# Kernel optimization log

Measured on AMD Instinct MI355X. Metric: run time of the kernel, lower is better.

The kernel has to match this reference:

```python
import jax, jax.numpy as jnp
import numpy as np

B, T, FBINS = 256, 512, 128
L1, L2, L3, NCLASS = 256, 256, 128, 10
Q_SCALE = 8.0  # 4-bit fixed point in [-1, 1]


def _quant(w):
    return jnp.clip(jnp.round(w * Q_SCALE) / Q_SCALE, -1.0, 1.0)


def qw(w):
    # straight-through quantizer (identity gradient)
    return w + jax.lax.stop_gradient(_quant(w) - w)


def egru_cell(x, h, W, b, H):
    # eGRU: 2-gate cell (update gate + candidate), softsign activations
    a = jnp.concatenate([x, h], axis=-1) @ qw(W).T + b  # [B, 2H]
    z = 0.5 * (jax.nn.soft_sign(a[:, :H]) + 1.0)
    h_cand = jax.nn.soft_sign(a[:, H:])
    return z * h + (1.0 - z) * h_cand


def setup_inputs() -> dict:
    key = jax.random.key(0)
    ks = jax.random.split(key, 8)
    s = lambda fan_in: 1.0 / np.sqrt(fan_in)
    return {
        "inputs": jax.random.normal(ks[0], (B, T, FBINS), jnp.float32),
        "h1_init": jax.random.uniform(ks[1], (B, L1), jnp.float32, -1.0, 1.0),
        "h2_init": jax.random.uniform(ks[2], (B, L2), jnp.float32, -1.0, 1.0),
        "W1": jax.random.normal(ks[3], (2 * L1, FBINS + L1), jnp.float32) * s(FBINS + L1),
        "b1": jnp.zeros((2 * L1,), jnp.float32),
        "W2": jax.random.normal(ks[4], (2 * L2, L1 + L2), jnp.float32) * s(L1 + L2),
        "b2": jnp.zeros((2 * L2,), jnp.float32),
        "W3": jax.random.normal(ks[5], (L3, L2), jnp.float32) * s(L2),
        "b3": jnp.zeros((L3,), jnp.float32),
        "W4": jax.random.normal(ks[6], (NCLASS, L3), jnp.float32) * s(L3),
        "b4": jnp.zeros((NCLASS,), jnp.float32),
    }


def reference(inputs, h1_init, h2_init, W1, b1, W2, b2, W3, b3, W4, b4):
    def step(carry, x_t):
        h1, h2 = carry
        h1 = egru_cell(x_t, h1, W1, b1, L1)
        h2 = egru_cell(h1, h2, W2, b2, L2)
        h3 = jnp.maximum(h2 @ qw(W3).T + b3, 0.0)  # clamp(min=0)
        h4 = h3 @ qw(W4).T + b4
        return (h1, h2), h4

    xs = jnp.swapaxes(inputs, 0, 1)  # [T, B, F]
    _, ys = jax.lax.scan(step, (h1_init, h2_init), xs)  # [T, B, C]
    y = jnp.swapaxes(ys, 0, 1)  # [B, T, C]
    return jax.nn.log_softmax(y, axis=-1)
```

## Files before the change

### kernel.cpp

```cpp
#include <hip/hip_runtime.h>

#define NT 512
#define FB 128
#define HD 256
#define NC 10
#define NG 32
#define GR 8

typedef __attribute__((ext_vector_type(8))) short bf16x8;
typedef __attribute__((ext_vector_type(4))) float f32x4;
typedef __attribute__((ext_vector_type(4))) unsigned u32x4;
typedef __attribute__((ext_vector_type(2))) unsigned u32x2;

static __device__ __forceinline__ short f2bf(float f){
  union { float f; unsigned u; } v; v.f = f;
  return (short)((v.u + 0x7fffu + ((v.u >> 16) & 1u)) >> 16);
}
static __device__ __forceinline__ float bf2f(short h){
  union { unsigned u; float f; } v; v.u = ((unsigned)(unsigned short)h) << 16;
  return v.f;
}
static __device__ __forceinline__ float quantw(float w){
  return fminf(fmaxf(rintf(w * 8.0f) * 0.125f, -1.0f), 1.0f);
}
static __device__ __forceinline__ bf16x8 loadqw8(const float* __restrict__ p){
  bf16x8 v;
#pragma unroll
  for (int j = 0; j < 8; ++j) v[j] = f2bf(quantw(p[j]));
  return v;
}
static __device__ __forceinline__ void split8(f32x4 a, f32x4 b, bf16x8& hi, bf16x8& lo){
  float v0[4] = {a[0],a[1],a[2],a[3]}, v1[4] = {b[0],b[1],b[2],b[3]};
#pragma unroll
  for (int j = 0; j < 4; ++j){
    short h = f2bf(v0[j]); hi[j] = h; lo[j] = f2bf(v0[j] - bf2f(h));
  }
#pragma unroll
  for (int j = 0; j < 4; ++j){
    short h = f2bf(v1[j]); hi[4+j] = h; lo[4+j] = f2bf(v1[j] - bf2f(h));
  }
}

static __device__ __forceinline__ void st_msg(unsigned* p, short hb, short lb, unsigned ep){
  u32x2 w;
  w[0] = (((unsigned)(unsigned short)hb) << 16) | ep;
  w[1] = (((unsigned)(unsigned short)lb) << 16) | ep;
  asm volatile("global_store_dwordx2 %0, %1, off sc1" :: "v"(p), "v"(w) : "memory");
}
static __device__ __forceinline__ void gather8(const unsigned* p, unsigned ep, bf16x8& hv, bf16x8& lv){
  u32x4 a, b, c, d;
  for (;;){
    asm volatile("global_load_dwordx4 %0, %4, off sc1\n\t"
                 "global_load_dwordx4 %1, %4, off offset:16 sc1\n\t"
                 "global_load_dwordx4 %2, %4, off offset:32 sc1\n\t"
                 "global_load_dwordx4 %3, %4, off offset:48 sc1\n\t"
                 "s_waitcnt vmcnt(0)"
                 : "=&v"(a), "=&v"(b), "=&v"(c), "=&v"(d) : "v"(p) : "memory");
    unsigned m = (a[0]^ep)|(a[1]^ep)|(a[2]^ep)|(a[3]^ep)
               | (b[0]^ep)|(b[1]^ep)|(b[2]^ep)|(b[3]^ep)
               | (c[0]^ep)|(c[1]^ep)|(c[2]^ep)|(c[3]^ep)
               | (d[0]^ep)|(d[1]^ep)|(d[2]^ep)|(d[3]^ep);
    if ((m & 0xffffu) == 0u) break;
  }
  hv[0]=(short)(a[0]>>16); lv[0]=(short)(a[1]>>16);
  hv[1]=(short)(a[2]>>16); lv[1]=(short)(a[3]>>16);
  hv[2]=(short)(b[0]>>16); lv[2]=(short)(b[1]>>16);
  hv[3]=(short)(b[2]>>16); lv[3]=(short)(b[3]>>16);
  hv[4]=(short)(c[0]>>16); lv[4]=(short)(c[1]>>16);
  hv[5]=(short)(c[2]>>16); lv[5]=(short)(c[3]>>16);
  hv[6]=(short)(d[0]>>16); lv[6]=(short)(d[1]>>16);
  hv[7]=(short)(d[2]>>16); lv[7]=(short)(d[3]>>16);
}

__global__ __launch_bounds__(256, 1)
void egru_persistent(const float* __restrict__ xg,
                     const float* __restrict__ h1ig, const float* __restrict__ h2ig,
                     const float* __restrict__ W1g, const float* __restrict__ b1g,
                     const float* __restrict__ W2g, const float* __restrict__ b2g,
                     const float* __restrict__ W3g, const float* __restrict__ b3g,
                     const float* __restrict__ W4g, const float* __restrict__ b4g,
                     float* __restrict__ outg, float* __restrict__ wsf)
{
  const int tid = threadIdx.x;
  const int gp  = blockIdx.x & 31;
  const int sb  = blockIdx.x >> 5;
  const int wv  = tid >> 6;
  const int ln  = tid & 15;
  const int lk  = (tid >> 4) & 3;
  const int rz  = sb * 32;
  const int lnl = 8 + (ln & 7);

  __shared__ __align__(16) short in1[16*384];
  __shared__ __align__(16) short in2[16*512];
  __shared__ float aldsA[64][17];
  __shared__ float aldsB[64][17];
  __shared__ float h1own[32][GR];
  __shared__ float h2own[32][GR];
  __shared__ float h3p[128], h3q[128], h3row[128];
  __shared__ float ytmp[16];
  __shared__ float W4L[10*130];
  __shared__ float b1s[64], b2s[64], b3L[128], b4L[10];

  unsigned* h1buf = reinterpret_cast<unsigned*>(wsf);
  unsigned* h2buf = h1buf + 262144;

  bf16x8 w1f[12], w2f[16], w3f[2][8];
  {
    const int arow = (wv < 2) ? (rz + wv*16 + ln) : (256 + rz + (wv-2)*16 + ln);
#pragma unroll
    for (int ks = 0; ks < 12; ++ks) w1f[ks] = loadqw8(W1g + arow*384 + ks*32 + lk*8);
#pragma unroll
    for (int ks = 0; ks < 16; ++ks) w2f[ks] = loadqw8(W2g + arow*512 + ks*32 + lk*8);
#pragma unroll
    for (int tl = 0; tl < 2; ++tl)
#pragma unroll
      for (int ks = 0; ks < 8; ++ks)
        w3f[tl][ks] = loadqw8(W3g + (wv*32 + tl*16 + ln)*256 + ks*32 + lk*8);
  }

  if (tid < 64){
    int grow = (tid < 32) ? (rz + tid) : (256 + rz + (tid - 32));
    b1s[tid] = b1g[grow];
    b2s[tid] = b2g[grow];
  }
  if (tid < 128) b3L[tid] = b3g[tid];
  if (tid < 10)  b4L[tid] = b4g[tid];
  for (int i = tid; i < 1280; i += 256)
    W4L[(i >> 7)*130 + (i & 127)] = quantw(W4g[i]);

  const int ur = tid >> 5, uc = tid & 31;
  {
    bf16x8 hv, lv;
    const float* p1 = h1ig + (size_t)(gp*GR + ur)*HD + uc*8;
    split8(*(const f32x4*)p1, *(const f32x4*)(p1+4), hv, lv);
    *(bf16x8*)((char*)in1 + ur*768       + ((256 + uc*16) ^ ((ur&7)<<4))) = hv;
    *(bf16x8*)((char*)in1 + (ur+8)*768   + ((256 + uc*16) ^ ((ur&7)<<4))) = lv;
    *(bf16x8*)((char*)in2 + ur*1024      + ((      uc*16) ^ ((ur&7)<<4))) = hv;
    *(bf16x8*)((char*)in2 + (ur+8)*1024  + ((      uc*16) ^ ((ur&7)<<4))) = lv;
    const float* p2 = h2ig + (size_t)(gp*GR + ur)*HD + uc*8;
    split8(*(const f32x4*)p2, *(const f32x4*)(p2+4), hv, lv);
    *(bf16x8*)((char*)in2 + ur*1024      + ((512 + uc*16) ^ ((ur&7)<<4))) = hv;
    *(bf16x8*)((char*)in2 + (ur+8)*1024  + ((512 + uc*16) ^ ((ur&7)<<4))) = lv;
    h1own[uc][ur] = h1ig[(size_t)(gp*GR+ur)*HD + rz + uc];
    h2own[uc][ur] = h2ig[(size_t)(gp*GR+ur)*HD + rz + uc];
  }
  const int xr = tid >> 4, xf = tid & 15;
  if (xr < 8){
    const float* px = xg + ((size_t)(gp*GR + xr)*NT + 0)*FB + xf*8;
    bf16x8 hv, lv;
    split8(*(const f32x4*)px, *(const f32x4*)(px+4), hv, lv);
    *(bf16x8*)((char*)in1 + xr*768     + ((xf*16) ^ ((xr&7)<<4))) = hv;
    *(bf16x8*)((char*)in1 + (xr+8)*768 + ((xf*16) ^ ((xr&7)<<4))) = lv;
  }
  __syncthreads();

  f32x4 acc1 = {0.f,0.f,0.f,0.f};
#pragma unroll
  for (int ks = 0; ks < 12; ++ks){
    bf16x8 bfr = *(bf16x8*)((char*)in1 + ln*768 + ((ks*64 + lk*16) ^ ((ln&7)<<4)));
    acc1 = __builtin_amdgcn_mfma_f32_16x16x32_bf16(w1f[ks], bfr, acc1, 0, 0, 0);
  }

  for (int t = 0; t < NT; ++t){
    unsigned* h1s = h1buf + (unsigned)(t & 1)*131072u + (unsigned)(gp*GR)*512u;
    unsigned* h2s = h2buf + (unsigned)(t & 1)*131072u + (unsigned)(gp*GR)*512u;
    unsigned* h2r = h2buf + (unsigned)((t + 1) & 1)*131072u + (unsigned)(gp*GR)*512u;

#pragma unroll
    for (int r4 = 0; r4 < 4; ++r4)
      aldsA[wv*16 + lk*4 + r4][ln] = acc1[r4];
    __syncthreads();
    {
      float az = aldsA[uc][ur]    + aldsA[uc][ur+8]    + b1s[uc];
      float ac = aldsA[32+uc][ur] + aldsA[32+uc][ur+8] + b1s[32+uc];
      float z  = 0.5f*(az/(1.0f+fabsf(az)) + 1.0f);
      float cd = ac/(1.0f+fabsf(ac));
      float hn = z*h1own[uc][ur] + (1.0f - z)*cd;
      h1own[uc][ur] = hn;
      short hb = f2bf(hn), lb = f2bf(hn - bf2f(hb));
      st_msg(&h1s[ur*512 + (rz + uc)*2], hb, lb, (unsigned)(t+1));
    }

    f32x4 xa = {0,0,0,0}, xb = {0,0,0,0};
    const bool pf = ((t+1) < NT) && (xr < 8);
    if (pf){
      const float* px = xg + ((size_t)(gp*GR + xr)*NT + (t+1))*FB + xf*8;
      xa = *(const f32x4*)px; xb = *(const f32x4*)(px+4);
    }

    if (t > 0){
      bf16x8 hv, lv;
      gather8(&h2r[ur*512 + uc*16], (unsigned)t, hv, lv);
      *(bf16x8*)((char*)in2 + ur*1024     + ((512 + uc*16) ^ ((ur&7)<<4))) = hv;
      *(bf16x8*)((char*)in2 + (ur+8)*1024 + ((512 + uc*16) ^ ((ur&7)<<4))) = lv;
    }
    if (pf){
      bf16x8 hv, lv;
      split8(xa, xb, hv, lv);
      *(bf16x8*)((char*)in1 + xr*768     + ((xf*16) ^ ((xr&7)<<4))) = hv;
      *(bf16x8*)((char*)in1 + (xr+8)*768 + ((xf*16) ^ ((xr&7)<<4))) = lv;
    }
    __syncthreads();

    f32x4 acc2 = {0.f,0.f,0.f,0.f};
#pragma unroll
    for (int ks = 8; ks < 16; ++ks){
      bf16x8 bfr = *(bf16x8*)((char*)in2 + ln*1024 + ((ks*64 + lk*16) ^ ((ln&7)<<4)));
      acc2 = __builtin_amdgcn_mfma_f32_16x16x32_bf16(w2f[ks], bfr, acc2, 0, 0, 0);
    }
    if (t > 0){
      f32x4 acc3a = {0,0,0,0}, acc3b = {0,0,0,0};
#pragma unroll
      for (int ks = 0; ks < 8; ++ks){
        bf16x8 bfr = *(bf16x8*)((char*)in2 + ln*1024 + ((512 + ks*64 + lk*16) ^ ((ln&7)<<4)));
        acc3a = __builtin_amdgcn_mfma_f32_16x16x32_bf16(w3f[0][ks], bfr, acc3a, 0, 0, 0);
        acc3b = __builtin_amdgcn_mfma_f32_16x16x32_bf16(w3f[1][ks], bfr, acc3b, 0, 0, 0);
      }
      if (ln == sb){
#pragma unroll
        for (int r4 = 0; r4 < 4; ++r4){
          int d0 = wv*32 + lk*4 + r4;
          h3p[d0] = acc3a[r4]; h3p[d0+16] = acc3b[r4];
        }
      }
      if (ln == sb + 8){
#pragma unroll
        for (int r4 = 0; r4 < 4; ++r4){
          int d0 = wv*32 + lk*4 + r4;
          h3q[d0] = acc3a[r4]; h3q[d0+16] = acc3b[r4];
        }
      }
      __syncthreads();
      if (tid < 128) h3row[tid] = fmaxf(h3p[tid] + h3q[tid] + b3L[tid], 0.0f);
      __syncthreads();
      if (wv == 0){
        const int l = tid, c = l >> 2, kq = l & 3;
        float p = 0.f;
        if (c < 10){
          const float* wr = &W4L[c*130 + kq*32];
          const float* hr = &h3row[kq*32];
#pragma unroll
          for (int k = 0; k < 32; ++k) p += wr[k]*hr[k];
        }
        p += __shfl_xor(p, 1, 4);
        p += __shfl_xor(p, 2, 4);
        if (c < 10 && kq == 0) ytmp[c] = p + b4L[c];
        asm volatile("s_waitcnt lgkmcnt(0)" ::: "memory");
        float yv = (l < 10) ? ytmp[l] : -INFINITY;
        float mx = yv;
#pragma unroll
        for (int off = 1; off < 16; off <<= 1)
          mx = fmaxf(mx, __shfl_xor(mx, off, 16));
        float ex = (l < 10) ? expf(yv - mx) : 0.0f;
        float sm = ex;
#pragma unroll
        for (int off = 1; off < 16; off <<= 1)
          sm += __shfl_xor(sm, off, 16);
        if (l < 10)
          outg[((size_t)(gp*GR + sb)*NT + (t-1))*NC + l] = yv - (mx + logf(sm));
      }
    }

    {
      bf16x8 hv, lv;
      gather8(&h1s[ur*512 + uc*16], (unsigned)(t+1), hv, lv);
      *(bf16x8*)((char*)in1 + ur*768      + ((256 + uc*16) ^ ((ur&7)<<4))) = hv;
      *(bf16x8*)((char*)in1 + (ur+8)*768  + ((256 + uc*16) ^ ((ur&7)<<4))) = lv;
      *(bf16x8*)((char*)in2 + ur*1024     + ((      uc*16) ^ ((ur&7)<<4))) = hv;
      *(bf16x8*)((char*)in2 + (ur+8)*1024 + ((      uc*16) ^ ((ur&7)<<4))) = lv;
    }
    __syncthreads();

#pragma unroll
    for (int ks = 0; ks < 8; ++ks){
      bf16x8 bfr = *(bf16x8*)((char*)in2 + ln*1024 + ((ks*64 + lk*16) ^ ((ln&7)<<4)));
      acc2 = __builtin_amdgcn_mfma_f32_16x16x32_bf16(w2f[ks], bfr, acc2, 0, 0, 0);
    }
#pragma unroll
    for (int r4 = 0; r4 < 4; ++r4)
      aldsB[wv*16 + lk*4 + r4][ln] = acc2[r4];
    __syncthreads();
    {
      float az = aldsB[uc][ur]    + aldsB[uc][ur+8]    + b2s[uc];
      float ac = aldsB[32+uc][ur] + aldsB[32+uc][ur+8] + b2s[32+uc];
      float z  = 0.5f*(az/(1.0f+fabsf(az)) + 1.0f);
      float cd = ac/(1.0f+fabsf(ac));
      float hn = z*h2own[uc][ur] + (1.0f - z)*cd;
      h2own[uc][ur] = hn;
      short hb = f2bf(hn), lb = f2bf(hn - bf2f(hb));
      st_msg(&h2s[ur*512 + (rz + uc)*2], hb, lb, (unsigned)(t+1));
    }

    if (t + 1 < NT){
      f32x4 a1n = {0.f,0.f,0.f,0.f};
#pragma unroll
      for (int ks = 0; ks < 12; ++ks){
        bf16x8 bfr = *(bf16x8*)((char*)in1 + ln*768 + ((ks*64 + lk*16) ^ ((ln&7)<<4)));
        a1n = __builtin_amdgcn_mfma_f32_16x16x32_bf16(w1f[ks], bfr, a1n, 0, 0, 0);
      }
      acc1 = a1n;
    }
  }

  {
    unsigned* h2e = h2buf + (unsigned)((NT-1) & 1)*131072u + (unsigned)(gp*GR)*512u;
    bf16x8 hv, lv;
    gather8(&h2e[ur*512 + uc*16], (unsigned)NT, hv, lv);
    *(bf16x8*)((char*)in2 + ur*1024     + ((512 + uc*16) ^ ((ur&7)<<4))) = hv;
    *(bf16x8*)((char*)in2 + (ur+8)*1024 + ((512 + uc*16) ^ ((ur&7)<<4))) = lv;
  }
  __syncthreads();
  {
    f32x4 acc3a = {0,0,0,0}, acc3b = {0,0,0,0};
#pragma unroll
    for (int ks = 0; ks < 8; ++ks){
      bf16x8 bfr = *(bf16x8*)((char*)in2 + ln*1024 + ((512 + ks*64 + lk*16) ^ ((ln&7)<<4)));
      acc3a = __builtin_amdgcn_mfma_f32_16x16x32_bf16(w3f[0][ks], bfr, acc3a, 0, 0, 0);
      acc3b = __builtin_amdgcn_mfma_f32_16x16x32_bf16(w3f[1][ks], bfr, acc3b, 0, 0, 0);
    }
    if (ln == sb){
#pragma unroll
      for (int r4 = 0; r4 < 4; ++r4){
        int d0 = wv*32 + lk*4 + r4;
        h3p[d0] = acc3a[r4]; h3p[d0+16] = acc3b[r4];
      }
    }
    if (ln == sb + 8){
#pragma unroll
      for (int r4 = 0; r4 < 4; ++r4){
        int d0 = wv*32 + lk*4 + r4;
        h3q[d0] = acc3a[r4]; h3q[d0+16] = acc3b[r4];
      }
    }
    __syncthreads();
    if (tid < 128) h3row[tid] = fmaxf(h3p[tid] + h3q[tid] + b3L[tid], 0.0f);
    __syncthreads();
    if (wv == 0){
      const int l = tid, c = l >> 2, kq = l & 3;
      float p = 0.f;
      if (c < 10){
        const float* wr = &W4L[c*130 + kq*32];
        const float* hr = &h3row[kq*32];
#pragma unroll
        for (int k = 0; k < 32; ++k) p += wr[k]*hr[k];
      }
      p += __shfl_xor(p, 1, 4);
      p += __shfl_xor(p, 2, 4);
      if (c < 10 && kq == 0) ytmp[c] = p + b4L[c];
      asm volatile("s_waitcnt lgkmcnt(0)" ::: "memory");
      float yv = (l < 10) ? ytmp[l] : -INFINITY;
      float mx = yv;
#pragma unroll
      for (int off = 1; off < 16; off <<= 1)
        mx = fmaxf(mx, __shfl_xor(mx, off, 16));
      float ex = (l < 10) ? expf(yv - mx) : 0.0f;
      float sm = ex;
#pragma unroll
      for (int off = 1; off < 16; off <<= 1)
        sm += __shfl_xor(sm, off, 16);
      if (l < 10)
        outg[((size_t)(gp*GR + sb)*NT + (NT-1))*NC + l] = yv - (mx + logf(sm));
    }
  }
}

extern "C" void kernel_launch(void* const* d_in, const int* in_sizes, int n_in,
                              void* d_out, int out_size, void* d_ws, size_t ws_size,
                              hipStream_t stream) {
  const float* xg  = (const float*)d_in[0];
  const float* h1i = (const float*)d_in[1];
  const float* h2i = (const float*)d_in[2];
  const float* W1  = (const float*)d_in[3];
  const float* b1  = (const float*)d_in[4];
  const float* W2  = (const float*)d_in[5];
  const float* b2  = (const float*)d_in[6];
  const float* W3  = (const float*)d_in[7];
  const float* b3  = (const float*)d_in[8];
  const float* W4  = (const float*)d_in[9];
  const float* b4  = (const float*)d_in[10];
  float* out = (float*)d_out;
  float* ws  = (float*)d_ws;

  hipMemsetAsync(d_ws, 0, 2u * 1024u * 1024u, stream);

  egru_persistent<<<dim3(256), dim3(256), 0, stream>>>(
      xg, h1i, h2i, W1, b1, W2, b2, W3, b3, W4, b4, out, ws);
}
```

Before: 1.904 ms.

## Issue cross-block hidden-state polls early and overlap with compute in persistent eGRU

The h2 and h1 message loads and the next-step x prefetch are now issued asynchronously ahead of use, with explicit vmcnt waits and a fallback spin loop if the epoch tags are not ready yet. This is meant to hide global-memory round-trip latency on the per-step critical path. Shared input buffers are split into separate x/h1/h2 arrays, h2 fragments are loaded once and reused for both W2 and W3 MFMAs, and h1 fragments are reused for the next W1 step. __syncthreads is replaced with a raw barrier macro and W4 LDS padding is changed, which adds reliance on hand-managed wait counts and scheduling barriers.

```diff
diff --git a/kernel.cpp b/kernel.cpp
--- a/kernel.cpp
+++ b/kernel.cpp
@@ -10,7 +10,6 @@
 typedef __attribute__((ext_vector_type(8))) short bf16x8;
 typedef __attribute__((ext_vector_type(4))) float f32x4;
 typedef __attribute__((ext_vector_type(4))) unsigned u32x4;
-typedef __attribute__((ext_vector_type(2))) unsigned u32x2;
 
 static __device__ __forceinline__ short f2bf(float f){
   union { float f; unsigned u; } v; v.f = f;
@@ -42,7 +41,7 @@
 }
 
 static __device__ __forceinline__ void st_msg(unsigned* p, short hb, short lb, unsigned ep){
-  u32x2 w;
+  __attribute__((ext_vector_type(2))) unsigned w;
   w[0] = (((unsigned)(unsigned short)hb) << 16) | ep;
   w[1] = (((unsigned)(unsigned short)lb) << 16) | ep;
   asm volatile("global_store_dwordx2 %0, %1, off sc1" :: "v"(p), "v"(w) : "memory");
@@ -71,6 +70,42 @@
   hv[6]=(short)(d[0]>>16); lv[6]=(short)(d[1]>>16);
   hv[7]=(short)(d[2]>>16); lv[7]=(short)(d[3]>>16);
 }
+static __device__ __forceinline__ bool chk_unpack(u32x4 a, u32x4 b, u32x4 c, u32x4 d,
+                                                  unsigned ep, bf16x8& hv, bf16x8& lv){
+  unsigned m = (a[0]^ep)|(a[1]^ep)|(a[2]^ep)|(a[3]^ep)
+             | (b[0]^ep)|(b[1]^ep)|(b[2]^ep)|(b[3]^ep)
+             | (c[0]^ep)|(c[1]^ep)|(c[2]^ep)|(c[3]^ep)
+             | (d[0]^ep)|(d[1]^ep)|(d[2]^ep)|(d[3]^ep);
+  if ((m & 0xffffu) != 0u) return false;
+  hv[0]=(short)(a[0]>>16); lv[0]=(short)(a[1]>>16);
+  hv[1]=(short)(a[2]>>16); lv[1]=(short)(a[3]>>16);
+  hv[2]=(short)(b[0]>>16); lv[2]=(short)(b[1]>>16);
+  hv[3]=(short)(b[2]>>16); lv[3]=(short)(b[3]>>16);
+  hv[4]=(short)(c[0]>>16); lv[4]=(short)(c[1]>>16);
+  hv[5]=(short)(c[2]>>16); lv[5]=(short)(c[3]>>16);
+  hv[6]=(short)(d[0]>>16); lv[6]=(short)(d[1]>>16);
+  hv[7]=(short)(d[2]>>16); lv[7]=(short)(d[3]>>16);
+  return true;
+}
+
+#define ISSUE_G8(P,A,B,C,D) \
+  asm volatile("global_load_dwordx4 %0, %4, off sc1\n\t" \
+               "global_load_dwordx4 %1, %4, off offset:16 sc1\n\t" \
+               "global_load_dwordx4 %2, %4, off offset:32 sc1\n\t" \
+               "global_load_dwordx4 %3, %4, off offset:48 sc1" \
+               : "=&v"(A),"=&v"(B),"=&v"(C),"=&v"(D) : "v"(P) : "memory")
+#define ISSUE_X2(P,A,B) \
+  asm volatile("global_load_dwordx4 %0, %2, off\n\t" \
+               "global_load_dwordx4 %1, %2, off offset:16" \
+               : "=&v"(A),"=&v"(B) : "v"(P) : "memory")
+#define WAITV4(N,A,B,C,D) do{ \
+  asm volatile("s_waitcnt vmcnt(" #N ")" : "+v"(A),"+v"(B),"+v"(C),"+v"(D) :: "memory"); \
+  __builtin_amdgcn_sched_barrier(0); }while(0)
+#define WAITV2(N,A,B) do{ \
+  asm volatile("s_waitcnt vmcnt(" #N ")" : "+v"(A),"+v"(B) :: "memory"); \
+  __builtin_amdgcn_sched_barrier(0); }while(0)
+#define BARRIER() do{ asm volatile("s_waitcnt lgkmcnt(0)" ::: "memory"); \
+  __builtin_amdgcn_s_barrier(); asm volatile("" ::: "memory"); }while(0)
 
 __global__ __launch_bounds__(256, 1)
 void egru_persistent(const float* __restrict__ xg,
@@ -88,17 +123,17 @@
   const int ln  = tid & 15;
   const int lk  = (tid >> 4) & 3;
   const int rz  = sb * 32;
-  const int lnl = 8 + (ln & 7);
-
-  __shared__ __align__(16) short in1[16*384];
-  __shared__ __align__(16) short in2[16*512];
+
+  __shared__ __align__(16) short inX [16*128];
+  __shared__ __align__(16) short inH1[16*256];
+  __shared__ __align__(16) short inH2[16*256];
   __shared__ float aldsA[64][17];
   __shared__ float aldsB[64][17];
   __shared__ float h1own[32][GR];
   __shared__ float h2own[32][GR];
   __shared__ float h3p[128], h3q[128], h3row[128];
   __shared__ float ytmp[16];
-  __shared__ float W4L[10*130];
+  __shared__ float W4L[1344];
   __shared__ float b1s[64], b2s[64], b3L[128], b4L[10];
 
   unsigned* h1buf = reinterpret_cast<unsigned*>(wsf);
@@ -125,22 +160,22 @@
   }
   if (tid < 128) b3L[tid] = b3g[tid];
   if (tid < 10)  b4L[tid] = b4g[tid];
-  for (int i = tid; i < 1280; i += 256)
-    W4L[(i >> 7)*130 + (i & 127)] = quantw(W4g[i]);
+  for (int i = tid; i < 1280; i += 256){
+    int c = i >> 7, k = i & 127;
+    W4L[c*134 + (k>>5)*33 + (k&31)] = quantw(W4g[i]);
+  }
 
   const int ur = tid >> 5, uc = tid & 31;
   {
     bf16x8 hv, lv;
     const float* p1 = h1ig + (size_t)(gp*GR + ur)*HD + uc*8;
     split8(*(const f32x4*)p1, *(const f32x4*)(p1+4), hv, lv);
-    *(bf16x8*)((char*)in1 + ur*768       + ((256 + uc*16) ^ ((ur&7)<<4))) = hv;
-    *(bf16x8*)((char*)in1 + (ur+8)*768   + ((256 + uc*16) ^ ((ur&7)<<4))) = lv;
-    *(bf16x8*)((char*)in2 + ur*1024      + ((      uc*16) ^ ((ur&7)<<4))) = hv;
-    *(bf16x8*)((char*)in2 + (ur+8)*1024  + ((      uc*16) ^ ((ur&7)<<4))) = lv;
+    *(bf16x8*)((char*)inH1 + ur*512     + ((uc*16) ^ ((ur&7)<<4))) = hv;
+    *(bf16x8*)((char*)inH1 + (ur+8)*512 + ((uc*16) ^ ((ur&7)<<4))) = lv;
     const float* p2 = h2ig + (size_t)(gp*GR + ur)*HD + uc*8;
     split8(*(const f32x4*)p2, *(const f32x4*)(p2+4), hv, lv);
-    *(bf16x8*)((char*)in2 + ur*1024      + ((512 + uc*16) ^ ((ur&7)<<4))) = hv;
-    *(bf16x8*)((char*)in2 + (ur+8)*1024  + ((512 + uc*16) ^ ((ur&7)<<4))) = lv;
+    *(bf16x8*)((char*)inH2 + ur*512     + ((uc*16) ^ ((ur&7)<<4))) = hv;
+    *(bf16x8*)((char*)inH2 + (ur+8)*512 + ((uc*16) ^ ((ur&7)<<4))) = lv;
     h1own[uc][ur] = h1ig[(size_t)(gp*GR+ur)*HD + rz + uc];
     h2own[uc][ur] = h2ig[(size_t)(gp*GR+ur)*HD + rz + uc];
   }
@@ -149,16 +184,21 @@
     const float* px = xg + ((size_t)(gp*GR + xr)*NT + 0)*FB + xf*8;
     bf16x8 hv, lv;
     split8(*(const f32x4*)px, *(const f32x4*)(px+4), hv, lv);
-    *(bf16x8*)((char*)in1 + xr*768     + ((xf*16) ^ ((xr&7)<<4))) = hv;
-    *(bf16x8*)((char*)in1 + (xr+8)*768 + ((xf*16) ^ ((xr&7)<<4))) = lv;
+    *(bf16x8*)((char*)inX + xr*256     + ((xf*16) ^ ((xr&7)<<4))) = hv;
+    *(bf16x8*)((char*)inX + (xr+8)*256 + ((xf*16) ^ ((xr&7)<<4))) = lv;
   }
   __syncthreads();
 
   f32x4 acc1 = {0.f,0.f,0.f,0.f};
 #pragma unroll
-  for (int ks = 0; ks < 12; ++ks){
-    bf16x8 bfr = *(bf16x8*)((char*)in1 + ln*768 + ((ks*64 + lk*16) ^ ((ln&7)<<4)));
-    acc1 = __builtin_amdgcn_mfma_f32_16x16x32_bf16(w1f[ks], bfr, acc1, 0, 0, 0);
+  for (int j = 0; j < 4; ++j){
+    bf16x8 fx = *(bf16x8*)((char*)inX + ln*256 + ((j*64 + lk*16) ^ ((ln&7)<<4)));
+    acc1 = __builtin_amdgcn_mfma_f32_16x16x32_bf16(w1f[j], fx, acc1, 0, 0, 0);
+  }
+#pragma unroll
+  for (int j = 0; j < 8; ++j){
+    bf16x8 fh = *(bf16x8*)((char*)inH1 + ln*512 + ((j*64 + lk*16) ^ ((ln&7)<<4)));
+    acc1 = __builtin_amdgcn_mfma_f32_16x16x32_bf16(w1f[4+j], fh, acc1, 0, 0, 0);
   }
 
   for (int t = 0; t < NT; ++t){
@@ -166,10 +206,13 @@
     unsigned* h2s = h2buf + (unsigned)(t & 1)*131072u + (unsigned)(gp*GR)*512u;
     unsigned* h2r = h2buf + (unsigned)((t + 1) & 1)*131072u + (unsigned)(gp*GR)*512u;
 
+    u32x4 g2a, g2b, g2c, g2d;
+    if (t > 0) ISSUE_G8(&h2r[ur*512 + uc*16], g2a, g2b, g2c, g2d);
+
 #pragma unroll
     for (int r4 = 0; r4 < 4; ++r4)
       aldsA[wv*16 + lk*4 + r4][ln] = acc1[r4];
-    __syncthreads();
+    BARRIER();
     {
       float az = aldsA[uc][ur]    + aldsA[uc][ur+8]    + b1s[uc];
       float ac = aldsA[32+uc][ur] + aldsA[32+uc][ur+8] + b1s[32+uc];
@@ -181,40 +224,41 @@
       st_msg(&h1s[ur*512 + (rz + uc)*2], hb, lb, (unsigned)(t+1));
     }
 
+    if (t > 0){
+      WAITV4(1, g2a, g2b, g2c, g2d);
+      bf16x8 hv, lv;
+      if (!chk_unpack(g2a, g2b, g2c, g2d, (unsigned)t, hv, lv))
+        gather8(&h2r[ur*512 + uc*16], (unsigned)t, hv, lv);
+      *(bf16x8*)((char*)inH2 + ur*512     + ((uc*16) ^ ((ur&7)<<4))) = hv;
+      *(bf16x8*)((char*)inH2 + (ur+8)*512 + ((uc*16) ^ ((ur&7)<<4))) = lv;
+    }
+
+    u32x4 g1a, g1b, g1c, g1d;
+    ISSUE_G8(&h1s[ur*512 + uc*16], g1a, g1b, g1c, g1d);
     f32x4 xa = {0,0,0,0}, xb = {0,0,0,0};
     const bool pf = ((t+1) < NT) && (xr < 8);
     if (pf){
       const float* px = xg + ((size_t)(gp*GR + xr)*NT + (t+1))*FB + xf*8;
-      xa = *(const f32x4*)px; xb = *(const f32x4*)(px+4);
-    }
-
-    if (t > 0){
-      bf16x8 hv, lv;
-      gather8(&h2r[ur*512 + uc*16], (unsigned)t, hv, lv);
-      *(bf16x8*)((char*)in2 + ur*1024     + ((512 + uc*16) ^ ((ur&7)<<4))) = hv;
-      *(bf16x8*)((char*)in2 + (ur+8)*1024 + ((512 + uc*16) ^ ((ur&7)<<4))) = lv;
-    }
-    if (pf){
-      bf16x8 hv, lv;
-      split8(xa, xb, hv, lv);
-      *(bf16x8*)((char*)in1 + xr*768     + ((xf*16) ^ ((xr&7)<<4))) = hv;
-      *(bf16x8*)((char*)in1 + (xr+8)*768 + ((xf*16) ^ ((xr&7)<<4))) = lv;
-    }
-    __syncthreads();
-
+      ISSUE_X2(px, xa, xb);
+    }
+    BARRIER();
+
+    bf16x8 fh2[8];
+#pragma unroll
+    for (int j = 0; j < 8; ++j)
+      fh2[j] = *(bf16x8*)((char*)inH2 + ln*512 + ((j*64 + lk*16) ^ ((ln&7)<<4)));
     f32x4 acc2 = {0.f,0.f,0.f,0.f};
 #pragma unroll
-    for (int ks = 8; ks < 16; ++ks){
-      bf16x8 bfr = *(bf16x8*)((char*)in2 + ln*1024 + ((ks*64 + lk*16) ^ ((ln&7)<<4)));
-      acc2 = __builtin_amdgcn_mfma_f32_16x16x32_bf16(w2f[ks], bfr, acc2, 0, 0, 0);
-    }
+    for (int j = 0; j < 8; ++j)
+      acc2 = __builtin_amdgcn_mfma_f32_16x16x32_bf16(w2f[8+j], fh2[j], acc2, 0, 0, 0);
+
+    float outv = 0.f; bool dow = false; size_t oaddr = 0;
     if (t > 0){
       f32x4 acc3a = {0,0,0,0}, acc3b = {0,0,0,0};
 #pragma unroll
-      for (int ks = 0; ks < 8; ++ks){
-        bf16x8 bfr = *(bf16x8*)((char*)in2 + ln*1024 + ((512 + ks*64 + lk*16) ^ ((ln&7)<<4)));
-        acc3a = __builtin_amdgcn_mfma_f32_16x16x32_bf16(w3f[0][ks], bfr, acc3a, 0, 0, 0);
-        acc3b = __builtin_amdgcn_mfma_f32_16x16x32_bf16(w3f[1][ks], bfr, acc3b, 0, 0, 0);
+      for (int j = 0; j < 8; ++j){
+        acc3a = __builtin_amdgcn_mfma_f32_16x16x32_bf16(w3f[0][j], fh2[j], acc3a, 0, 0, 0);
+        acc3b = __builtin_amdgcn_mfma_f32_16x16x32_bf16(w3f[1][j], fh2[j], acc3b, 0, 0, 0);
       }
       if (ln == sb){
 #pragma unroll
@@ -230,14 +274,14 @@
           h3q[d0] = acc3a[r4]; h3q[d0+16] = acc3b[r4];
         }
       }
-      __syncthreads();
+      BARRIER();
       if (tid < 128) h3row[tid] = fmaxf(h3p[tid] + h3q[tid] + b3L[tid], 0.0f);
-      __syncthreads();
+      BARRIER();
       if (wv == 0){
         const int l = tid, c = l >> 2, kq = l & 3;
         float p = 0.f;
         if (c < 10){
-          const float* wr = &W4L[c*130 + kq*32];
+          const float* wr = &W4L[c*134 + kq*33];
           const float* hr = &h3row[kq*32];
 #pragma unroll
           for (int k = 0; k < 32; ++k) p += wr[k]*hr[k];
@@ -256,30 +300,36 @@
 #pragma unroll
         for (int off = 1; off < 16; off <<= 1)
           sm += __shfl_xor(sm, off, 16);
-        if (l < 10)
-          outg[((size_t)(gp*GR + sb)*NT + (t-1))*NC + l] = yv - (mx + logf(sm));
+        if (l < 10){
+          outv = yv - (mx + logf(sm));
+          dow = true;
+          oaddr = ((size_t)(gp*GR + sb)*NT + (t-1))*NC + l;
+        }
       }
     }
 
     {
+      WAITV4(2, g1a, g1b, g1c, g1d);
       bf16x8 hv, lv;
-      gather8(&h1s[ur*512 + uc*16], (unsigned)(t+1), hv, lv);
-      *(bf16x8*)((char*)in1 + ur*768      + ((256 + uc*16) ^ ((ur&7)<<4))) = hv;
-      *(bf16x8*)((char*)in1 + (ur+8)*768  + ((256 + uc*16) ^ ((ur&7)<<4))) = lv;
-      *(bf16x8*)((char*)in2 + ur*1024     + ((      uc*16) ^ ((ur&7)<<4))) = hv;
-      *(bf16x8*)((char*)in2 + (ur+8)*1024 + ((      uc*16) ^ ((ur&7)<<4))) = lv;
-    }
-    __syncthreads();
-
-#pragma unroll
-    for (int ks = 0; ks < 8; ++ks){
-      bf16x8 bfr = *(bf16x8*)((char*)in2 + ln*1024 + ((ks*64 + lk*16) ^ ((ln&7)<<4)));
-      acc2 = __builtin_amdgcn_mfma_f32_16x16x32_bf16(w2f[ks], bfr, acc2, 0, 0, 0);
-    }
+      if (!chk_unpack(g1a, g1b, g1c, g1d, (unsigned)(t+1), hv, lv))
+        gather8(&h1s[ur*512 + uc*16], (unsigned)(t+1), hv, lv);
+      *(bf16x8*)((char*)inH1 + ur*512     + ((uc*16) ^ ((ur&7)<<4))) = hv;
+      *(bf16x8*)((char*)inH1 + (ur+8)*512 + ((uc*16) ^ ((ur&7)<<4))) = lv;
+    }
+    if (dow) outg[oaddr] = outv;
+    BARRIER();
+
+    bf16x8 fh1[8];
+#pragma unroll
+    for (int j = 0; j < 8; ++j)
+      fh1[j] = *(bf16x8*)((char*)inH1 + ln*512 + ((j*64 + lk*16) ^ ((ln&7)<<4)));
+#pragma unroll
+    for (int j = 0; j < 8; ++j)
+      acc2 = __builtin_amdgcn_mfma_f32_16x16x32_bf16(w2f[j], fh1[j], acc2, 0, 0, 0);
 #pragma unroll
     for (int r4 = 0; r4 < 4; ++r4)
       aldsB[wv*16 + lk*4 + r4][ln] = acc2[r4];
-    __syncthreads();
+    BARRIER();
     {
       float az = aldsB[uc][ur]    + aldsB[uc][ur+8]    + b2s[uc];
       float ac = aldsB[32+uc][ur] + aldsB[32+uc][ur+8] + b2s[32+uc];
@@ -291,13 +341,25 @@
       st_msg(&h2s[ur*512 + (rz + uc)*2], hb, lb, (unsigned)(t+1));
     }
 
+    WAITV2(1, xa, xb);
+    if (pf){
+      bf16x8 hv, lv;
+      split8(xa, xb, hv, lv);
+      *(bf16x8*)((char*)inX + xr*256     + ((xf*16) ^ ((xr&7)<<4))) = hv;
+      *(bf16x8*)((char*)inX + (xr+8)*256 + ((xf*16) ^ ((xr&7)<<4))) = lv;
+    }
+    BARRIER();
+
     if (t + 1 < NT){
       f32x4 a1n = {0.f,0.f,0.f,0.f};
 #pragma unroll
-      for (int ks = 0; ks < 12; ++ks){
-        bf16x8 bfr = *(bf16x8*)((char*)in1 + ln*768 + ((ks*64 + lk*16) ^ ((ln&7)<<4)));
-        a1n = __builtin_amdgcn_mfma_f32_16x16x32_bf16(w1f[ks], bfr, a1n, 0, 0, 0);
-      }
+      for (int j = 0; j < 4; ++j){
+        bf16x8 fx = *(bf16x8*)((char*)inX + ln*256 + ((j*64 + lk*16) ^ ((ln&7)<<4)));
+        a1n = __builtin_amdgcn_mfma_f32_16x16x32_bf16(w1f[j], fx, a1n, 0, 0, 0);
+      }
+#pragma unroll
+      for (int j = 0; j < 8; ++j)
+        a1n = __builtin_amdgcn_mfma_f32_16x16x32_bf16(w1f[4+j], fh1[j], a1n, 0, 0, 0);
       acc1 = a1n;
     }
   }
@@ -306,17 +368,20 @@
     unsigned* h2e = h2buf + (unsigned)((NT-1) & 1)*131072u + (unsigned)(gp*GR)*512u;
     bf16x8 hv, lv;
     gather8(&h2e[ur*512 + uc*16], (unsigned)NT, hv, lv);
-    *(bf16x8*)((char*)in2 + ur*1024     + ((512 + uc*16) ^ ((ur&7)<<4))) = hv;
-    *(bf16x8*)((char*)in2 + (ur+8)*1024 + ((512 + uc*16) ^ ((ur&7)<<4))) = lv;
-  }
-  __syncthreads();
+    *(bf16x8*)((char*)inH2 + ur*512     + ((uc*16) ^ ((ur&7)<<4))) = hv;
+    *(bf16x8*)((char*)inH2 + (ur+8)*512 + ((uc*16) ^ ((ur&7)<<4))) = lv;
+  }
+  BARRIER();
   {
+    bf16x8 fh2[8];
+#pragma unroll
+    for (int j = 0; j < 8; ++j)
+      fh2[j] = *(bf16x8*)((char*)inH2 + ln*512 + ((j*64 + lk*16) ^ ((ln&7)<<4)));
     f32x4 acc3a = {0,0,0,0}, acc3b = {0,0,0,0};
 #pragma unroll
-    for (int ks = 0; ks < 8; ++ks){
-      bf16x8 bfr = *(bf16x8*)((char*)in2 + ln*1024 + ((512 + ks*64 + lk*16) ^ ((ln&7)<<4)));
-      acc3a = __builtin_amdgcn_mfma_f32_16x16x32_bf16(w3f[0][ks], bfr, acc3a, 0, 0, 0);
-      acc3b = __builtin_amdgcn_mfma_f32_16x16x32_bf16(w3f[1][ks], bfr, acc3b, 0, 0, 0);
+    for (int j = 0; j < 8; ++j){
+      acc3a = __builtin_amdgcn_mfma_f32_16x16x32_bf16(w3f[0][j], fh2[j], acc3a, 0, 0, 0);
+      acc3b = __builtin_amdgcn_mfma_f32_16x16x32_bf16(w3f[1][j], fh2[j], acc3b, 0, 0, 0);
     }
     if (ln == sb){
 #pragma unroll
@@ -332,14 +397,14 @@
         h3q[d0] = acc3a[r4]; h3q[d0+16] = acc3b[r4];
       }
     }
-    __syncthreads();
+    BARRIER();
     if (tid < 128) h3row[tid] = fmaxf(h3p[tid] + h3q[tid] + b3L[tid], 0.0f);
-    __syncthreads();
+    BARRIER();
     if (wv == 0){
       const int l = tid, c = l >> 2, kq = l & 3;
       float p = 0.f;
       if (c < 10){
-        const float* wr = &W4L[c*130 + kq*32];
+        const float* wr = &W4L[c*134 + kq*33];
         const float* hr = &h3row[kq*32];
 #pragma unroll
         for (int k = 0; k < 32; ++k) p += wr[k]*hr[k];
```

Measured after the change: 1.808 ms. 5.0% less time.
